# Kernel tuning notes

Measured on AMD Instinct MI355X. Metric: run time of the kernel, lower is better.

The kernel has to match this reference:

```python
import jax, jax.numpy as jnp
import numpy as np

N = 100000        # num nodes
E = 3_200_000     # num edges
NFEAT, NHID, NCLASS = 256, 128, 40
BN_EPS = 1e-5


def _gcn_norm(edge_index, edge_weight, num_nodes):
    """PyG gcn_norm with self-loops (fill value 1.0): returns (src, dst, norm)."""
    loop = jnp.arange(num_nodes)
    src = jnp.concatenate([edge_index[0], loop])
    dst = jnp.concatenate([edge_index[1], loop])
    ew = jnp.concatenate([edge_weight, jnp.ones((num_nodes,), edge_weight.dtype)])
    deg = jax.ops.segment_sum(ew, dst, num_segments=num_nodes)
    dinv = jnp.where(deg > 0, jax.lax.rsqrt(jnp.maximum(deg, 1e-30)), 0.0)
    norm = dinv[src] * ew * dinv[dst]  # [E+N]
    return src, dst, norm


def _gcn_layer(h, W, b, src, dst, norm, num_nodes):
    lin = h @ W                                   # [N, out]
    msg = lin[src] * norm[:, None]                # gather + scale  [E+N, out]
    agg = jax.ops.segment_sum(msg, dst, num_segments=num_nodes)
    return agg + b


def _bn(h, gamma, beta):
    # BatchNorm1d in training mode: biased batch statistics
    m = jnp.mean(h, axis=0)
    v = jnp.mean(jnp.square(h - m), axis=0)
    return (h - m) * jax.lax.rsqrt(v + BN_EPS) * gamma + beta


def setup_inputs() -> dict:
    key = jax.random.key(0)
    ks = jax.random.split(key, 12)
    s_in = 1.0 / np.sqrt(NFEAT)
    s_h = 1.0 / np.sqrt(NHID)
    return {
        "x": jax.random.normal(ks[0], (N, NFEAT), jnp.float32),
        "edge_index": jax.random.randint(ks[1], (2, E), 0, N, dtype=jnp.int32),
        "edge_weight": jax.random.uniform(ks[2], (E,), jnp.float32),
        "W1": jax.random.normal(ks[3], (NFEAT, NHID), jnp.float32) * s_in,
        "b1": jnp.zeros((NHID,), jnp.float32),
        "g1": jnp.ones((NHID,), jnp.float32),
        "beta1": jnp.zeros((NHID,), jnp.float32),
        "W2": jax.random.normal(ks[4], (NHID, NHID), jnp.float32) * s_h,
        "b2": jnp.zeros((NHID,), jnp.float32),
        "g2": jnp.ones((NHID,), jnp.float32),
        "beta2": jnp.zeros((NHID,), jnp.float32),
        "W3": jax.random.normal(ks[5], (NHID, NHID), jnp.float32) * s_h,
        "b3": jnp.zeros((NHID,), jnp.float32),
        "g3": jnp.ones((NHID,), jnp.float32),
        "beta3": jnp.zeros((NHID,), jnp.float32),
        "linW": jax.random.normal(ks[6], (3 * NHID, NCLASS), jnp.float32) / np.sqrt(3 * NHID),
        "linb": jnp.zeros((NCLASS,), jnp.float32),
    }


def reference(x, edge_index, edge_weight,
              W1, b1, g1, beta1,
              W2, b2, g2, beta2,
              W3, b3, g3, beta3,
              linW, linb):
    src, dst, norm = _gcn_norm(edge_index, edge_weight, N)
    x1 = _bn(jax.nn.relu(_gcn_layer(x, W1, b1, src, dst, norm, N)), g1, beta1)
    x2 = _bn(jax.nn.relu(_gcn_layer(x1, W2, b2, src, dst, norm, N)), g2, beta2)
    x3 = _bn(_gcn_layer(x2, W3, b3, src, dst, norm, N), g3, beta3)  # note: no relu on x3
    embed_x = jnp.concatenate([x1, x2, x3], axis=1)  # [N, 3*NHID]
    logits = embed_x @ linW + linb                   # [N, NCLASS]
    return logits, jax.nn.softmax(logits, axis=1), embed_x
```

## Files before the change

### kernel.cpp

```cpp
#include <hip/hip_runtime.h>
#include <hip/hip_bf16.h>
#include <hip/hip_fp16.h>
#include <math.h>

#define NN 100000
#define NE 3200000
#define NF 256
#define NH 128
#define NC 40
#define BN_EPS 1e-5f

typedef __attribute__((ext_vector_type(8))) short bf16x8;
typedef __attribute__((ext_vector_type(4))) float f32x4;

__device__ __forceinline__ float2 bf2_unpack(unsigned int v) {
    return make_float2(__uint_as_float(v << 16), __uint_as_float(v & 0xffff0000u));
}
__device__ __forceinline__ unsigned int pack2bf(float lo, float hi) {
    unsigned int a = (unsigned int)__hip_bfloat16_raw(__float2bfloat16(lo)).x;
    unsigned int b = (unsigned int)__hip_bfloat16_raw(__float2bfloat16(hi)).x;
    return a | (b << 16);
}
__device__ __forceinline__ float4 affine4(float4 v, float4 sc, float4 sh) {
    v.x = fmaf(v.x, sc.x, sh.x);
    v.y = fmaf(v.y, sc.y, sh.y);
    v.z = fmaf(v.z, sc.z, sh.z);
    v.w = fmaf(v.w, sc.w, sh.w);
    return v;
}

__global__ __launch_bounds__(256) void k_init(unsigned long long* hist, float* sums) {
    int i = blockIdx.x * 256 + threadIdx.x;
    if (i < NN) hist[i] = 0ULL;
    if (i < 3 * 1024) sums[i] = 0.0f;
}

__global__ __launch_bounds__(256) void k_edge(const int* __restrict__ ei, const float* __restrict__ ew,
                                              unsigned long long* __restrict__ hist,
                                              int* __restrict__ pos) {
    int e = blockIdx.x * 256 + threadIdx.x;
    if (e >= NE) return;
    int d = __builtin_nontemporal_load(&ei[NE + e]);
    float w = __builtin_nontemporal_load(&ew[e]);
    unsigned long long pack = (1ULL << 44) | (unsigned long long)(w * 4294967296.0f);
    unsigned long long old = atomicAdd(&hist[d], pack);
    __builtin_nontemporal_store((int)(old >> 44), &pos[e]);
}

__global__ __launch_bounds__(1024) void k_scan(const unsigned long long* __restrict__ hist,
                                               int* __restrict__ rowptr,
                                               float* __restrict__ dinv) {
    __shared__ int wsum[16];
    __shared__ int s_carry;
    int t = threadIdx.x;
    int lane = t & 63, wid = t >> 6;
    if (t == 0) s_carry = 0;
    __syncthreads();
    for (int base = 0; base < NN; base += 4096) {
        int i0 = base + t * 4;
        int c[4];
#pragma unroll
        for (int j = 0; j < 4; j++) {
            int i = i0 + j;
            unsigned long long h = (i < NN) ? hist[i] : 0ULL;
            c[j] = (int)(h >> 44);
            if (i < NN) {
                float ws = (float)(h & 0xFFFFFFFFFFFULL) * 2.3283064365386963e-10f;
                dinv[i] = rsqrtf(1.0f + ws);
            }
        }
        int v = c[0] + c[1] + c[2] + c[3];
        int x = v;
#pragma unroll
        for (int off = 1; off < 64; off <<= 1) {
            int y = __shfl_up(x, off);
            if (lane >= off) x += y;
        }
        if (lane == 63) wsum[wid] = x;
        __syncthreads();
        if (wid == 0 && lane < 16) {
            int s = wsum[lane];
#pragma unroll
            for (int off = 1; off < 16; off <<= 1) {
                int y = __shfl_up(s, off);
                if (lane >= off) s += y;
            }
            wsum[lane] = s;
        }
        __syncthreads();
        int woff = (wid > 0) ? wsum[wid - 1] : 0;
        int incl = x + woff;
        int carry = s_carry;
        int run = carry + incl - v;
#pragma unroll
        for (int j = 0; j < 4; j++) {
            int i = i0 + j;
            if (i < NN) rowptr[i] = run;
            run += c[j];
        }
        __syncthreads();
        if (t == 1023) s_carry = carry + incl;
        __syncthreads();
    }
    if (t == 0) rowptr[NN] = s_carry;
}

__global__ __launch_bounds__(256) void k_scatter(const int* __restrict__ ei, const float* __restrict__ ew,
                                                 const float* __restrict__ dinv,
                                                 const int* __restrict__ rowptr,
                                                 const int* __restrict__ pos,
                                                 unsigned int* __restrict__ cw) {
    int e = blockIdx.x * 256 + threadIdx.x;
    if (e >= NE) return;
    int s = __builtin_nontemporal_load(&ei[e]);
    int d = __builtin_nontemporal_load(&ei[NE + e]);
    float w = __builtin_nontemporal_load(&ew[e]);
    float nv = dinv[s] * w * dinv[d];
    unsigned int h = (unsigned int)__half_as_ushort(__float2half(nv)) & 0x7fffu;
    unsigned int packed = (unsigned int)s | (h << 17);
    int p = __builtin_nontemporal_load(&pos[e]);
    __builtin_nontemporal_store(packed, &cw[rowptr[d] + p]);
}

template <int K, bool BN>
__device__ __forceinline__ void gemm_body(unsigned int (*Bt)[20], const float* H, float* Hw,
                                          const float* scsh, int ldh, const float* W,
                                          __hip_bfloat16* out, int blk, int t) {
    int wid = t >> 6, l = t & 63;
    int l15 = l & 15, lhi = l >> 4;
    int rowbase = blk * 128 + wid * 32;
    int ar0 = rowbase + l15;      if (ar0 >= NN) ar0 = NN - 1;
    int ar1 = rowbase + 16 + l15; if (ar1 >= NN) ar1 = NN - 1;

    f32x4 acc[2][8];
#pragma unroll
    for (int rt = 0; rt < 2; rt++)
#pragma unroll
        for (int ct = 0; ct < 8; ct++) acc[rt][ct] = (f32x4){0.f, 0.f, 0.f, 0.f};

    for (int kb = 0; kb < K / 32; kb++) {
        __syncthreads();
        for (int i = t; i < 2048; i += 256) {
            int c = i & 127, k2l = i >> 7;
            int k = kb * 32 + 2 * k2l;
            Bt[c][k2l] = pack2bf(W[(size_t)k * NH + c], W[(size_t)(k + 1) * NH + c]);
        }
        __syncthreads();
        int kk = kb * 32 + lhi * 8;
        const float4* a0p = (const float4*)&H[(size_t)ar0 * ldh + kk];
        const float4* a1p = (const float4*)&H[(size_t)ar1 * ldh + kk];
        float4 x0 = a0p[0], x1 = a0p[1];
        float4 y0 = a1p[0], y1 = a1p[1];
        if constexpr (BN) {
            float4 sc0 = *(const float4*)&scsh[kk];
            float4 sc1 = *(const float4*)&scsh[kk + 4];
            float4 sh0 = *(const float4*)&scsh[128 + kk];
            float4 sh1 = *(const float4*)&scsh[128 + kk + 4];
            x0 = affine4(x0, sc0, sh0); x1 = affine4(x1, sc1, sh1);
            y0 = affine4(y0, sc0, sh0); y1 = affine4(y1, sc1, sh1);
            *(float4*)&Hw[(size_t)ar0 * ldh + kk] = x0;
            *(float4*)&Hw[(size_t)ar0 * ldh + kk + 4] = x1;
            *(float4*)&Hw[(size_t)ar1 * ldh + kk] = y0;
            *(float4*)&Hw[(size_t)ar1 * ldh + kk + 4] = y1;
        }
        union { unsigned int u[4]; bf16x8 v; } af0, af1;
        af0.u[0] = pack2bf(x0.x, x0.y); af0.u[1] = pack2bf(x0.z, x0.w);
        af0.u[2] = pack2bf(x1.x, x1.y); af0.u[3] = pack2bf(x1.z, x1.w);
        af1.u[0] = pack2bf(y0.x, y0.y); af1.u[1] = pack2bf(y0.z, y0.w);
        af1.u[2] = pack2bf(y1.x, y1.y); af1.u[3] = pack2bf(y1.z, y1.w);
#pragma unroll
        for (int ct = 0; ct < 8; ct++) {
            bf16x8 b = *(const bf16x8*)&Bt[ct * 16 + l15][lhi * 4];
            acc[0][ct] = __builtin_amdgcn_mfma_f32_16x16x32_bf16(af0.v, b, acc[0][ct], 0, 0, 0);
            acc[1][ct] = __builtin_amdgcn_mfma_f32_16x16x32_bf16(af1.v, b, acc[1][ct], 0, 0, 0);
        }
    }
#pragma unroll
    for (int rt = 0; rt < 2; rt++)
#pragma unroll
        for (int ct = 0; ct < 8; ct++)
#pragma unroll
            for (int reg = 0; reg < 4; reg++) {
                int row = rowbase + rt * 16 + lhi * 4 + reg;
                if (row < NN)
                    out[(size_t)row * NH + ct * 16 + l15] = __float2bfloat16(acc[rt][ct][reg]);
            }
}

__global__ __launch_bounds__(256) void k_gemm1(const float* __restrict__ H,
                                               const float* __restrict__ W,
                                               __hip_bfloat16* __restrict__ out) {
    __shared__ unsigned int Bt[128][20];
    gemm_body<NF, false>(Bt, H, nullptr, nullptr, NF, W, out, (int)blockIdx.x, (int)threadIdx.x);
}

__global__ __launch_bounds__(256) void k_gemm_bn(const float* H, float* Hw,
                                                 const float* __restrict__ scsh,
                                                 const float* __restrict__ W,
                                                 __hip_bfloat16* __restrict__ out) {
    __shared__ unsigned int Bt[128][20];
    gemm_body<NH, true>(Bt, H, Hw, scsh, 384, W, out, (int)blockIdx.x, (int)threadIdx.x);
}

__global__ __launch_bounds__(256) void k_agg(const unsigned int* __restrict__ linb,
                                             const float* __restrict__ dinv,
                                             const int* __restrict__ rowptr,
                                             const unsigned int* __restrict__ cw,
                                             const float* __restrict__ bias,
                                             float* __restrict__ outp, int do_relu) {
    int t = threadIdx.x;
    int node = blockIdx.x * 4 + (t >> 6);
    if (node >= NN) return;
    int ch = t & 63;
    int c = ch << 1;
    float di = dinv[node];
    float2 sv = bf2_unpack(linb[(size_t)node * 64 + ch]);
    float a0 = fmaf(sv.x, di * di, bias[c]);
    float a1 = fmaf(sv.y, di * di, bias[c + 1]);
    int beg = rowptr[node], end = rowptr[node + 1];
    int j = beg;
    for (; j + 16 <= end; j += 16) {
        unsigned int pk[16];
#pragma unroll
        for (int q = 0; q < 16; q++) pk[q] = cw[j + q];
        unsigned int v[16];
#pragma unroll
        for (int q = 0; q < 16; q++) v[q] = linb[(size_t)(pk[q] & 0x1FFFFu) * 64 + ch];
#pragma unroll
        for (int q = 0; q < 16; q++) {
            float w = __half2float(__ushort_as_half((unsigned short)(pk[q] >> 17)));
            float2 f = bf2_unpack(v[q]);
            a0 = fmaf(f.x, w, a0);
            a1 = fmaf(f.y, w, a1);
        }
    }
    for (; j + 4 <= end; j += 4) {
        unsigned int pk[4];
#pragma unroll
        for (int q = 0; q < 4; q++) pk[q] = cw[j + q];
        unsigned int v[4];
#pragma unroll
        for (int q = 0; q < 4; q++) v[q] = linb[(size_t)(pk[q] & 0x1FFFFu) * 64 + ch];
#pragma unroll
        for (int q = 0; q < 4; q++) {
            float w = __half2float(__ushort_as_half((unsigned short)(pk[q] >> 17)));
            float2 f = bf2_unpack(v[q]);
            a0 = fmaf(f.x, w, a0);
            a1 = fmaf(f.y, w, a1);
        }
    }
    for (; j < end; j++) {
        unsigned int pk = cw[j];
        unsigned int vv = linb[(size_t)(pk & 0x1FFFFu) * 64 + ch];
        float w = __half2float(__ushort_as_half((unsigned short)(pk >> 17)));
        float2 f = bf2_unpack(vv);
        a0 = fmaf(f.x, w, a0);
        a1 = fmaf(f.y, w, a1);
    }
    if (do_relu) { a0 = fmaxf(a0, 0.f); a1 = fmaxf(a1, 0.f); }
    *(float2*)&outp[(size_t)node * 384 + c] = make_float2(a0, a1);
}

__global__ __launch_bounds__(256) void k_stats(const float* __restrict__ pre, float* __restrict__ sums) {
    int t = threadIdx.x;
    int c = t & 127, h = t >> 7;
    float s = 0.f, s2 = 0.f;
    for (int r = blockIdx.x * 2 + h; r < NN; r += gridDim.x * 2) {
        float v = pre[(size_t)r * 384 + c];
        s += v;
        s2 = fmaf(v, v, s2);
    }
    __shared__ float ls[256], ls2[256];
    ls[t] = s; ls2[t] = s2;
    __syncthreads();
    if (t < 128) {
        atomicAdd(&sums[c], ls[t] + ls[t + 128]);
        atomicAdd(&sums[NH + c], ls2[t] + ls2[t + 128]);
    }
}

__global__ void k_bnfinal(float* __restrict__ sums, const float* __restrict__ g,
                          const float* __restrict__ beta) {
    int c = threadIdx.x;
    if (c < NH) {
        float m = sums[c] * (1.0f / NN);
        float v = sums[NH + c] * (1.0f / NN) - m * m;
        float rstd = rsqrtf(v + BN_EPS);
        float sc = g[c] * rstd;
        sums[256 + c] = sc;
        sums[384 + c] = beta[c] - m * sc;
    }
}

__global__ __launch_bounds__(256) void k_final(const float* __restrict__ embed, float* embedW,
                                               const float* __restrict__ scsh3,
                                               const float* __restrict__ linW,
                                               const float* __restrict__ linb,
                                               float* __restrict__ logits, float* __restrict__ probs) {
    __shared__ unsigned int Wt[3 * 16 * 196];
    int t = threadIdx.x;
    for (int i = t; i < 3 * 16 * 192; i += 256) {
        int ct = i / (16 * 192);
        int rem = i - ct * (16 * 192);
        int c = rem / 192, k2 = rem - c * 192;
        int col = ct * 16 + c;
        float lo = (col < NC) ? linW[(size_t)(2 * k2) * NC + col] : 0.f;
        float hi = (col < NC) ? linW[(size_t)(2 * k2 + 1) * NC + col] : 0.f;
        Wt[(ct * 16 + c) * 196 + k2] = pack2bf(lo, hi);
    }
    __syncthreads();

    int wid = t >> 6, l = t & 63;
    int rowbase = blockIdx.x * 64 + wid * 16;
    int l15 = l & 15, lhi = l >> 4;

    int arow = rowbase + l15;
    if (arow > NN - 1) arow = NN - 1;
    const float4* ap = (const float4*)&embed[(size_t)arow * 384 + lhi * 8];

    f32x4 acc0 = {0.f, 0.f, 0.f, 0.f};
    f32x4 acc1 = {0.f, 0.f, 0.f, 0.f};
    f32x4 acc2 = {0.f, 0.f, 0.f, 0.f};

    for (int kb = 0; kb < 12; kb++) {
        float4 a0 = ap[kb * 8];
        float4 a1 = ap[kb * 8 + 1];
        if (kb >= 8) {
            int kk = kb * 32 + lhi * 8 - 256;
            float4 sc0 = *(const float4*)&scsh3[kk];
            float4 sc1 = *(const float4*)&scsh3[kk + 4];
            float4 sh0 = *(const float4*)&scsh3[128 + kk];
            float4 sh1 = *(const float4*)&scsh3[128 + kk + 4];
            a0 = affine4(a0, sc0, sh0);
            a1 = affine4(a1, sc1, sh1);
            *(float4*)&embedW[(size_t)arow * 384 + kb * 32 + lhi * 8] = a0;
            *(float4*)&embedW[(size_t)arow * 384 + kb * 32 + lhi * 8 + 4] = a1;
        }
        union { unsigned int u[4]; bf16x8 v; } af;
        af.u[0] = pack2bf(a0.x, a0.y);
        af.u[1] = pack2bf(a0.z, a0.w);
        af.u[2] = pack2bf(a1.x, a1.y);
        af.u[3] = pack2bf(a1.z, a1.w);
        int wbase = kb * 16 + lhi * 4;
        bf16x8 b0 = *(const bf16x8*)&Wt[(0 * 16 + l15) * 196 + wbase];
        bf16x8 b1 = *(const bf16x8*)&Wt[(1 * 16 + l15) * 196 + wbase];
        bf16x8 b2 = *(const bf16x8*)&Wt[(2 * 16 + l15) * 196 + wbase];
        acc0 = __builtin_amdgcn_mfma_f32_16x16x32_bf16(af.v, b0, acc0, 0, 0, 0);
        acc1 = __builtin_amdgcn_mfma_f32_16x16x32_bf16(af.v, b1, acc1, 0, 0, 0);
        acc2 = __builtin_amdgcn_mfma_f32_16x16x32_bf16(af.v, b2, acc2, 0, 0, 0);
    }

    int col0 = 0 * 16 + l15, col1 = 1 * 16 + l15, col2 = 2 * 16 + l15;
    float lb0 = (col0 < NC) ? linb[col0] : 0.f;
    float lb1 = (col1 < NC) ? linb[col1] : 0.f;
    float lb2 = (col2 < NC) ? linb[col2] : 0.f;

#pragma unroll
    for (int reg = 0; reg < 4; reg++) {
        int row = rowbase + lhi * 4 + reg;
        float v0 = acc0[reg] + lb0;
        float v1 = acc1[reg] + lb1;
        float v2 = acc2[reg] + lb2;
        float m = fmaxf(v0, v1);
        if (col2 < NC) m = fmaxf(m, v2);
#pragma unroll
        for (int off = 1; off < 16; off <<= 1) m = fmaxf(m, __shfl_xor(m, off));
        float e0 = __expf(v0 - m);
        float e1 = __expf(v1 - m);
        float e2 = (col2 < NC) ? __expf(v2 - m) : 0.f;
        float s = e0 + e1 + e2;
#pragma unroll
        for (int off = 1; off < 16; off <<= 1) s += __shfl_xor(s, off);
        float inv = 1.0f / s;
        if (row < NN) {
            size_t base = (size_t)row * NC;
            logits[base + col0] = v0;
            probs[base + col0] = e0 * inv;
            logits[base + col1] = v1;
            probs[base + col1] = e1 * inv;
            if (col2 < NC) {
                logits[base + col2] = v2;
                probs[base + col2] = e2 * inv;
            }
        }
    }
}

extern "C" void kernel_launch(void* const* d_in, const int* in_sizes, int n_in,
                              void* d_out, int out_size, void* d_ws, size_t ws_size,
                              hipStream_t stream) {
    const float* x    = (const float*)d_in[0];
    const int*   ei   = (const int*)d_in[1];
    const float* ew   = (const float*)d_in[2];
    const float* W1   = (const float*)d_in[3];
    const float* b1   = (const float*)d_in[4];
    const float* g1   = (const float*)d_in[5];
    const float* be1  = (const float*)d_in[6];
    const float* W2   = (const float*)d_in[7];
    const float* b2   = (const float*)d_in[8];
    const float* g2   = (const float*)d_in[9];
    const float* be2  = (const float*)d_in[10];
    const float* W3   = (const float*)d_in[11];
    const float* b3   = (const float*)d_in[12];
    const float* g3   = (const float*)d_in[13];
    const float* be3  = (const float*)d_in[14];
    const float* linW = (const float*)d_in[15];
    const float* linb = (const float*)d_in[16];

    float* out    = (float*)d_out;
    float* logits = out;
    float* probs  = out + (size_t)NN * NC;
    float* embed  = out + (size_t)2 * NN * NC;

    char* ws = (char*)d_ws;
    size_t off = 0;
    auto alloc = [&](size_t bytes) -> char* {
        char* p = ws + off;
        off = (off + bytes + 255) & ~(size_t)255;
        return p;
    };
    float*              dinv   = (float*)alloc((size_t)NN * 4);
    unsigned long long* hist   = (unsigned long long*)alloc((size_t)NN * 8);
    int*                rowptr = (int*)alloc((size_t)(NN + 1) * 4);
    unsigned int*       cw     = (unsigned int*)alloc((size_t)NE * 4);
    __hip_bfloat16*     lin    = (__hip_bfloat16*)alloc((size_t)NN * NH * 2);
    int*                pos    = (int*)alloc((size_t)NE * 4);
    float*              sums   = (float*)alloc(3 * 1024 * 4);
    (void)ws_size; (void)in_sizes; (void)n_in; (void)out_size;

    int gN = (NN + 255) / 256;
    int gE = (NE + 255) / 256;
    int gM = (NN + 127) / 128;
    int gA = (NN + 3) / 4;
    int gF = (NN + 63) / 64;

    k_init<<<gN, 256, 0, stream>>>(hist, sums);
    k_edge<<<gE, 256, 0, stream>>>(ei, ew, hist, pos);
    k_scan<<<1, 1024, 0, stream>>>(hist, rowptr, dinv);
    k_scatter<<<gE, 256, 0, stream>>>(ei, ew, dinv, rowptr, pos, cw);

    k_gemm1<<<gM, 256, 0, stream>>>(x, W1, lin);
    k_agg<<<gA, 256, 0, stream>>>((const unsigned int*)lin, dinv, rowptr, cw, b1, embed + 0, 1);
    k_stats<<<1024, 256, 0, stream>>>(embed + 0, sums + 0);
    k_bnfinal<<<1, 128, 0, stream>>>(sums + 0, g1, be1);
    k_gemm_bn<<<gM, 256, 0, stream>>>(embed + 0, embed + 0, sums + 256, W2, lin);
    k_agg<<<gA, 256, 0, stream>>>((const unsigned int*)lin, dinv, rowptr, cw, b2, embed + 128, 1);
    k_stats<<<1024, 256, 0, stream>>>(embed + 128, sums + 1024);
    k_bnfinal<<<1, 128, 0, stream>>>(sums + 1024, g2, be2);
    k_gemm_bn<<<gM, 256, 0, stream>>>(embed + 128, embed + 128, sums + 1024 + 256, W3, lin);
    k_agg<<<gA, 256, 0, stream>>>((const unsigned int*)lin, dinv, rowptr, cw, b3, embed + 256, 0);
    k_stats<<<1024, 256, 0, stream>>>(embed + 256, sums + 2048);
    k_bnfinal<<<1, 128, 0, stream>>>(sums + 2048, g3, be3);
    k_final<<<gF, 256, 0, stream>>>(embed, embed, sums + 2048 + 256, linW, linb, logits, probs);
}
```

Baseline: 1.028 ms.

## Parallelize CSR scan, fuse BN finalize into consumers, pack weight into pos

Replaces the single-block serial prefix scan over node degrees with a three-kernel multi-block scan (block partials, partial scan, local scan). Folds the BatchNorm scale/shift computation into the GEMM and final kernels, removing three tiny launches. Stores the edge weight as fp16 alongside the slot index in pos, so the scatter kernel no longer re-reads edge_weight; this adds fp16 rounding of the raw weight. Also guards writes for out-of-range rows.

New measurement: 947.9 us (median of 2 runs). 1.09x faster.

```diff
diff --git a/kernel.cpp b/kernel.cpp
--- a/kernel.cpp
+++ b/kernel.cpp
@@ -9,6 +9,7 @@
 #define NH 128
 #define NC 40
 #define BN_EPS 1e-5f
+#define NB 98
 
 typedef __attribute__((ext_vector_type(8))) short bf16x8;
 typedef __attribute__((ext_vector_type(4))) float f32x4;
@@ -37,98 +38,118 @@
 
 __global__ __launch_bounds__(256) void k_edge(const int* __restrict__ ei, const float* __restrict__ ew,
                                               unsigned long long* __restrict__ hist,
-                                              int* __restrict__ pos) {
+                                              unsigned int* __restrict__ pos) {
     int e = blockIdx.x * 256 + threadIdx.x;
     if (e >= NE) return;
     int d = __builtin_nontemporal_load(&ei[NE + e]);
     float w = __builtin_nontemporal_load(&ew[e]);
     unsigned long long pack = (1ULL << 44) | (unsigned long long)(w * 4294967296.0f);
     unsigned long long old = atomicAdd(&hist[d], pack);
-    __builtin_nontemporal_store((int)(old >> 44), &pos[e]);
-}
-
-__global__ __launch_bounds__(1024) void k_scan(const unsigned long long* __restrict__ hist,
-                                               int* __restrict__ rowptr,
+    unsigned int h16 = (unsigned int)__half_as_ushort(__float2half(w));
+    __builtin_nontemporal_store((unsigned int)(old >> 44) | (h16 << 16), &pos[e]);
+}
+
+__global__ __launch_bounds__(256) void k_scanA(const unsigned long long* __restrict__ hist,
+                                               int* __restrict__ partial,
                                                float* __restrict__ dinv) {
-    __shared__ int wsum[16];
-    __shared__ int s_carry;
+    __shared__ int ws[4];
+    int t = threadIdx.x;
+    int i0 = blockIdx.x * 1024 + t * 4;
+    int s = 0;
+#pragma unroll
+    for (int j = 0; j < 4; j++) {
+        int i = i0 + j;
+        if (i < NN) {
+            unsigned long long h = hist[i];
+            s += (int)(h >> 44);
+            float wsum = (float)(h & 0xFFFFFFFFFFFULL) * 2.3283064365386963e-10f;
+            dinv[i] = rsqrtf(1.0f + wsum);
+        }
+    }
+#pragma unroll
+    for (int off = 32; off >= 1; off >>= 1) s += __shfl_xor(s, off);
+    if ((t & 63) == 0) ws[t >> 6] = s;
+    __syncthreads();
+    if (t == 0) partial[blockIdx.x] = ws[0] + ws[1] + ws[2] + ws[3];
+}
+
+__global__ void k_scanB(int* __restrict__ partial, int* __restrict__ rowptr) {
+    __shared__ int buf[128];
+    int t = threadIdx.x;
+    buf[t] = (t < NB) ? partial[t] : 0;
+    __syncthreads();
+    if (t == 0) {
+        int r = 0;
+        for (int b = 0; b < NB; b++) { int v = buf[b]; buf[b] = r; r += v; }
+        rowptr[NN] = r;
+    }
+    __syncthreads();
+    if (t < NB) partial[t] = buf[t];
+}
+
+__global__ __launch_bounds__(256) void k_scanC(const unsigned long long* __restrict__ hist,
+                                               const int* __restrict__ partial,
+                                               int* __restrict__ rowptr) {
+    __shared__ int wsum[4];
     int t = threadIdx.x;
     int lane = t & 63, wid = t >> 6;
-    if (t == 0) s_carry = 0;
-    __syncthreads();
-    for (int base = 0; base < NN; base += 4096) {
-        int i0 = base + t * 4;
-        int c[4];
-#pragma unroll
-        for (int j = 0; j < 4; j++) {
-            int i = i0 + j;
-            unsigned long long h = (i < NN) ? hist[i] : 0ULL;
-            c[j] = (int)(h >> 44);
-            if (i < NN) {
-                float ws = (float)(h & 0xFFFFFFFFFFFULL) * 2.3283064365386963e-10f;
-                dinv[i] = rsqrtf(1.0f + ws);
-            }
-        }
-        int v = c[0] + c[1] + c[2] + c[3];
-        int x = v;
-#pragma unroll
-        for (int off = 1; off < 64; off <<= 1) {
-            int y = __shfl_up(x, off);
-            if (lane >= off) x += y;
-        }
-        if (lane == 63) wsum[wid] = x;
-        __syncthreads();
-        if (wid == 0 && lane < 16) {
-            int s = wsum[lane];
-#pragma unroll
-            for (int off = 1; off < 16; off <<= 1) {
-                int y = __shfl_up(s, off);
-                if (lane >= off) s += y;
-            }
-            wsum[lane] = s;
-        }
-        __syncthreads();
-        int woff = (wid > 0) ? wsum[wid - 1] : 0;
-        int incl = x + woff;
-        int carry = s_carry;
-        int run = carry + incl - v;
-#pragma unroll
-        for (int j = 0; j < 4; j++) {
-            int i = i0 + j;
-            if (i < NN) rowptr[i] = run;
-            run += c[j];
-        }
-        __syncthreads();
-        if (t == 1023) s_carry = carry + incl;
-        __syncthreads();
-    }
-    if (t == 0) rowptr[NN] = s_carry;
-}
-
-__global__ __launch_bounds__(256) void k_scatter(const int* __restrict__ ei, const float* __restrict__ ew,
+    int i0 = blockIdx.x * 1024 + t * 4;
+    int c[4];
+#pragma unroll
+    for (int j = 0; j < 4; j++) {
+        int i = i0 + j;
+        c[j] = (i < NN) ? (int)(hist[i] >> 44) : 0;
+    }
+    int v = c[0] + c[1] + c[2] + c[3];
+    int x = v;
+#pragma unroll
+    for (int off = 1; off < 64; off <<= 1) {
+        int y = __shfl_up(x, off);
+        if (lane >= off) x += y;
+    }
+    if (lane == 63) wsum[wid] = x;
+    __syncthreads();
+    if (t == 0) {
+        int r = 0;
+#pragma unroll
+        for (int w2 = 0; w2 < 4; w2++) { int s = wsum[w2]; wsum[w2] = r; r += s; }
+    }
+    __syncthreads();
+    int start = partial[blockIdx.x] + wsum[wid] + x - v;
+#pragma unroll
+    for (int j = 0; j < 4; j++) {
+        int i = i0 + j;
+        if (i < NN) rowptr[i] = start;
+        start += c[j];
+    }
+}
+
+__global__ __launch_bounds__(256) void k_scatter(const int* __restrict__ ei,
                                                  const float* __restrict__ dinv,
                                                  const int* __restrict__ rowptr,
-                                                 const int* __restrict__ pos,
+                                                 const unsigned int* __restrict__ pos,
                                                  unsigned int* __restrict__ cw) {
     int e = blockIdx.x * 256 + threadIdx.x;
     if (e >= NE) return;
     int s = __builtin_nontemporal_load(&ei[e]);
     int d = __builtin_nontemporal_load(&ei[NE + e]);
-    float w = __builtin_nontemporal_load(&ew[e]);
+    unsigned int pw = __builtin_nontemporal_load(&pos[e]);
+    float w = __half2float(__ushort_as_half((unsigned short)(pw >> 16)));
     float nv = dinv[s] * w * dinv[d];
     unsigned int h = (unsigned int)__half_as_ushort(__float2half(nv)) & 0x7fffu;
     unsigned int packed = (unsigned int)s | (h << 17);
-    int p = __builtin_nontemporal_load(&pos[e]);
-    __builtin_nontemporal_store(packed, &cw[rowptr[d] + p]);
+    __builtin_nontemporal_store(packed, &cw[rowptr[d] + (int)(pw & 0xFFFFu)]);
 }
 
 template <int K, bool BN>
 __device__ __forceinline__ void gemm_body(unsigned int (*Bt)[20], const float* H, float* Hw,
-                                          const float* scsh, int ldh, const float* W,
-                                          __hip_bfloat16* out, int blk, int t) {
+                                          const float* scp, const float* shp, int ldh,
+                                          const float* W, __hip_bfloat16* out, int blk, int t) {
     int wid = t >> 6, l = t & 63;
     int l15 = l & 15, lhi = l >> 4;
     int rowbase = blk * 128 + wid * 32;
+    bool ok0 = (rowbase + l15) < NN;
+    bool ok1 = (rowbase + 16 + l15) < NN;
     int ar0 = rowbase + l15;      if (ar0 >= NN) ar0 = NN - 1;
     int ar1 = rowbase + 16 + l15; if (ar1 >= NN) ar1 = NN - 1;
 
@@ -152,16 +173,20 @@
         float4 x0 = a0p[0], x1 = a0p[1];
         float4 y0 = a1p[0], y1 = a1p[1];
         if constexpr (BN) {
-            float4 sc0 = *(const float4*)&scsh[kk];
-            float4 sc1 = *(const float4*)&scsh[kk + 4];
-            float4 sh0 = *(const float4*)&scsh[128 + kk];
-            float4 sh1 = *(const float4*)&scsh[128 + kk + 4];
+            float4 sc0 = *(const float4*)&scp[kk];
+            float4 sc1 = *(const float4*)&scp[kk + 4];
+            float4 sh0 = *(const float4*)&shp[kk];
+            float4 sh1 = *(const float4*)&shp[kk + 4];
             x0 = affine4(x0, sc0, sh0); x1 = affine4(x1, sc1, sh1);
             y0 = affine4(y0, sc0, sh0); y1 = affine4(y1, sc1, sh1);
-            *(float4*)&Hw[(size_t)ar0 * ldh + kk] = x0;
-            *(float4*)&Hw[(size_t)ar0 * ldh + kk + 4] = x1;
-            *(float4*)&Hw[(size_t)ar1 * ldh + kk] = y0;
-            *(float4*)&Hw[(size_t)ar1 * ldh + kk + 4] = y1;
+            if (ok0) {
+                *(float4*)&Hw[(size_t)ar0 * ldh + kk] = x0;
+                *(float4*)&Hw[(size_t)ar0 * ldh + kk + 4] = x1;
+            }
+            if (ok1) {
+                *(float4*)&Hw[(size_t)ar1 * ldh + kk] = y0;
+                *(float4*)&Hw[(size_t)ar1 * ldh + kk + 4] = y1;
+            }
         }
         union { unsigned int u[4]; bf16x8 v; } af0, af1;
         af0.u[0] = pack2bf(x0.x, x0.y); af0.u[1] = pack2bf(x0.z, x0.w);
@@ -191,15 +216,29 @@
                                                const float* __restrict__ W,
                                                __hip_bfloat16* __restrict__ out) {
     __shared__ unsigned int Bt[128][20];
-    gemm_body<NF, false>(Bt, H, nullptr, nullptr, NF, W, out, (int)blockIdx.x, (int)threadIdx.x);
+    gemm_body<NF, false>(Bt, H, nullptr, nullptr, nullptr, NF, W, out, (int)blockIdx.x, (int)threadIdx.x);
 }
 
 __global__ __launch_bounds__(256) void k_gemm_bn(const float* H, float* Hw,
-                                                 const float* __restrict__ scsh,
+                                                 const float* __restrict__ sums,
+                                                 const float* __restrict__ g,
+                                                 const float* __restrict__ beta,
                                                  const float* __restrict__ W,
                                                  __hip_bfloat16* __restrict__ out) {
     __shared__ unsigned int Bt[128][20];
-    gemm_body<NH, true>(Bt, H, Hw, scsh, 384, W, out, (int)blockIdx.x, (int)threadIdx.x);
+    __shared__ __align__(16) float scL[128];
+    __shared__ __align__(16) float shL[128];
+    int t = threadIdx.x;
+    if (t < 128) {
+        float m = sums[t] * (1.0f / NN);
+        float v = sums[NH + t] * (1.0f / NN) - m * m;
+        float r = rsqrtf(v + BN_EPS);
+        float sc = g[t] * r;
+        scL[t] = sc;
+        shL[t] = beta[t] - m * sc;
+    }
+    __syncthreads();
+    gemm_body<NH, true>(Bt, H, Hw, scL, shL, 384, W, out, (int)blockIdx.x, (int)threadIdx.x);
 }
 
 __global__ __launch_bounds__(256) void k_agg(const unsigned int* __restrict__ linb,
@@ -279,26 +318,25 @@
     }
 }
 
-__global__ void k_bnfinal(float* __restrict__ sums, const float* __restrict__ g,
-                          const float* __restrict__ beta) {
-    int c = threadIdx.x;
-    if (c < NH) {
-        float m = sums[c] * (1.0f / NN);
-        float v = sums[NH + c] * (1.0f / NN) - m * m;
-        float rstd = rsqrtf(v + BN_EPS);
-        float sc = g[c] * rstd;
-        sums[256 + c] = sc;
-        sums[384 + c] = beta[c] - m * sc;
-    }
-}
-
 __global__ __launch_bounds__(256) void k_final(const float* __restrict__ embed, float* embedW,
-                                               const float* __restrict__ scsh3,
+                                               const float* __restrict__ sums3,
+                                               const float* __restrict__ g3,
+                                               const float* __restrict__ be3,
                                                const float* __restrict__ linW,
                                                const float* __restrict__ linb,
                                                float* __restrict__ logits, float* __restrict__ probs) {
     __shared__ unsigned int Wt[3 * 16 * 196];
-    int t = threadIdx.x;
+    __shared__ __align__(16) float scL[128];
+    __shared__ __align__(16) float shL[128];
+    int t = threadIdx.x;
+    if (t < 128) {
+        float m = sums3[t] * (1.0f / NN);
+        float v = sums3[NH + t] * (1.0f / NN) - m * m;
+        float r = rsqrtf(v + BN_EPS);
+        float sc = g3[t] * r;
+        scL[t] = sc;
+        shL[t] = be3[t] - m * sc;
+    }
     for (int i = t; i < 3 * 16 * 192; i += 256) {
         int ct = i / (16 * 192);
         int rem = i - ct * (16 * 192);
@@ -314,6 +352,7 @@
     int rowbase = blockIdx.x * 64 + wid * 16;
     int l15 = l & 15, lhi = l >> 4;
 
+    bool okA = (rowbase + l15) < NN;
     int arow = rowbase + l15;
     if (arow > NN - 1) arow = NN - 1;
     const float4* ap = (const float4*)&embed[(size_t)arow * 384 + lhi * 8];
@@ -327,14 +366,16 @@
         float4 a1 = ap[kb * 8 + 1];
         if (kb >= 8) {
             int kk = kb * 32 + lhi * 8 - 256;
-            float4 sc0 = *(const float4*)&scsh3[kk];
-            float4 sc1 = *(const float4*)&scsh3[kk + 4];
-            float4 sh0 = *(const float4*)&scsh3[128 + kk];
-            float4 sh1 = *(const float4*)&scsh3[128 + kk + 4];
+            float4 sc0 = *(const float4*)&scL[kk];
+            float4 sc1 = *(const float4*)&scL[kk + 4];
+            float4 sh0 = *(const float4*)&shL[kk];
+            float4 sh1 = *(const float4*)&shL[kk + 4];
             a0 = affine4(a0, sc0, sh0);
             a1 = affine4(a1, sc1, sh1);
-            *(float4*)&embedW[(size_t)arow * 384 + kb * 32 + lhi * 8] = a0;
-            *(float4*)&embedW[(size_t)arow * 384 + kb * 32 + lhi * 8 + 4] = a1;
+            if (okA) {
+                *(float4*)&embedW[(size_t)arow * 384 + kb * 32 + lhi * 8] = a0;
+                *(float4*)&embedW[(size_t)arow * 384 + kb * 32 + lhi * 8 + 4] = a1;
+            }
         }
         union { unsigned int u[4]; bf16x8 v; } af;
         af.u[0] = pack2bf(a0.x, a0.y);
@@ -419,13 +460,14 @@
         off = (off + bytes + 255) & ~(size_t)255;
         return p;
     };
-    float*              dinv   = (float*)alloc((size_t)NN * 4);
-    unsigned long long* hist   = (unsigned long long*)alloc((size_t)NN * 8);
-    int*                rowptr = (int*)alloc((size_t)(NN + 1) * 4);
-    unsigned int*       cw     = (unsigned int*)alloc((size_t)NE * 4);
-    __hip_bfloat16*     lin    = (__hip_bfloat16*)alloc((size_t)NN * NH * 2);
-    int*                pos    = (int*)alloc((size_t)NE * 4);
-    float*              sums   = (float*)alloc(3 * 1024 * 4);
+    float*              dinv    = (float*)alloc((size_t)NN * 4);
+    unsigned long long* hist    = (unsigned long long*)alloc((size_t)NN * 8);
+    int*                rowptr  = (int*)alloc((size_t)(NN + 1) * 4);
+    int*                partial = (int*)alloc(128 * 4);
+    unsigned int*       cw      = (unsigned int*)alloc((size_t)NE * 4);
+    __hip_bfloat16*     lin     = (__hip_bfloat16*)alloc((size_t)NN * NH * 2);
+    unsigned int*       pos     = (unsigned int*)alloc((size_t)NE * 4);
+    float*              sums    = (float*)alloc(3 * 1024 * 4);
     (void)ws_size; (void)in_sizes; (void)n_in; (void)out_size;
 
     int gN = (NN + 255) / 256;
@@ -436,20 +478,19 @@
 
     k_init<<<gN, 256, 0, stream>>>(hist, sums);
     k_edge<<<gE, 256, 0, stream>>>(ei, ew, hist, pos);
-    k_scan<<<1, 1024, 0, stream>>>(hist, rowptr, dinv);
-    k_scatter<<<gE, 256, 0, stream>>>(ei, ew, dinv, rowptr, pos, cw);
+    k_scanA<<<NB, 256, 0, stream>>>(hist, partial, dinv);
+    k_scanB<<<1, 128, 0, stream>>>(partial, rowptr);
+    k_scanC<<<NB, 256, 0, stream>>>(hist, partial, rowptr);
+    k_scatter<<<gE, 256, 0, stream>>>(ei, dinv, rowptr, pos, cw);
 
     k_gemm1<<<gM, 256, 0, stream>>>(x, W1, lin);
     k_agg<<<gA, 256, 0, stream>>>((const unsigned int*)lin, dinv, rowptr, cw, b1, embed + 0, 1);
     k_stats<<<1024, 256, 0, stream>>>(embed + 0, sums + 0);
-    k_bnfinal<<<1, 128, 0, stream>>>(sums + 0, g1, be1);
-    k_gemm_bn<<<gM, 256, 0, stream>>>(embed + 0, embed + 0, sums + 256, W2, lin);
+    k_gemm_bn<<<gM, 256, 0, stream>>>(embed + 0, embed + 0, sums + 0, g1, be1, W2, lin);
     k_agg<<<gA, 256, 0, stream>>>((const unsigned int*)lin, dinv, rowptr, cw, b2, embed + 128, 1);
     k_stats<<<1024, 256, 0, stream>>>(embed + 128, sums + 1024);
-    k_bnfinal<<<1, 128, 0, stream>>>(sums + 1024, g2, be2);
-    k_gemm_bn<<<gM, 256, 0, stream>>>(embed + 128, embed + 128, sums + 1024 + 256, W3, lin);
+    k_gemm_bn<<<gM, 256, 0, stream>>>(embed + 128, embed + 128, sums + 1024, g2, be2, W3, lin);
     k_agg<<<gA, 256, 0, stream>>>((const unsigned int*)lin, dinv, rowptr, cw, b3, embed + 256, 0);
     k_stats<<<1024, 256, 0, stream>>>(embed + 256, sums + 2048);
-    k_bnfinal<<<1, 128, 0, stream>>>(sums + 2048, g3, be3);
-    k_final<<<gF, 256, 0, stream>>>(embed, embed, sums + 2048 + 256, linW, linb, logits, probs);
-}
+    k_final<<<gF, 256, 0, stream>>>(embed, embed, sums + 2048, g3, be3, linW, linb, logits, probs);
+}
```
